# Optimization experiments

Measured on AMD Instinct MI355X. Metric: run time of the kernel, lower is better.

## Reference

```python
import jax, jax.numpy as jnp
import numpy as np

PAD_IDX = 0  # tgt_dict.stoi[PAD_WORD]
TLEN, BATCH, SLEN, CVOCAB = 64, 32, 128, 64
D, VOCAB = 1024, 50257


def setup_inputs() -> dict:
    key = jax.random.key(0)
    ks = jax.random.split(key, 7)
    hidden = jax.random.normal(ks[0], (TLEN * BATCH, D), dtype=jnp.float32)
    # attention distribution over source positions (rows sum to 1)
    attn = jax.nn.softmax(jax.random.normal(ks[1], (TLEN * BATCH, SLEN), dtype=jnp.float32), axis=-1)
    # sparse one-hot indicator: each source position maps to one extended-vocab slot
    src_idx = jax.random.randint(ks[2], (SLEN, BATCH), 0, CVOCAB)
    src_map = jax.nn.one_hot(src_idx, CVOCAB, dtype=jnp.float32)  # [slen, batch, cvocab]
    W_gen = jax.random.normal(ks[3], (VOCAB, D), dtype=jnp.float32) * 0.02
    b_gen = jnp.zeros((VOCAB,), dtype=jnp.float32)
    W_copy = jax.random.normal(ks[4], (1, D), dtype=jnp.float32) * 0.02
    b_copy = jnp.zeros((1,), dtype=jnp.float32)
    return {"hidden": hidden, "attn": attn, "src_map": src_map,
            "W_gen": W_gen, "b_gen": b_gen, "W_copy": W_copy, "b_copy": b_copy}


def reference(hidden, attn, src_map, W_gen, b_gen, W_copy, b_copy):
    slen, batch, cvocab = src_map.shape
    # p_softmax over tgt dict, with PAD masked to -inf before softmax
    logits = hidden @ W_gen.T + b_gen                      # [N, vocab]
    logits = logits.at[:, PAD_IDX].set(-jnp.inf)
    prob = jax.nn.softmax(logits, axis=-1)                 # [N, vocab]
    # copy gate p(z)
    p_copy = jax.nn.sigmoid(hidden @ W_copy.T + b_copy)    # [N, 1]
    out_prob = prob * (1.0 - p_copy)                       # [N, vocab]
    mul_attn = attn * p_copy                               # [N, slen]
    # torch flattening is tlen-major: view(-1, batch, slen) -> [tlen, batch, slen]
    mul_attn = mul_attn.reshape(-1, batch, slen)
    # bmm against sparse one-hot indicator: [tlen,batch,slen] x [slen,batch,cvocab]
    copy_prob = jnp.einsum('tbs,sbc->tbc', mul_attn, src_map)
    copy_prob = copy_prob.reshape(-1, cvocab)              # [N, cvocab]
    return jnp.concatenate([out_prob, copy_prob], axis=1)  # [N, vocab+cvocab]
```

## Files before the change

### kernel.cpp

```cpp
#include <hip/hip_runtime.h>
#include <hip/hip_bf16.h>

#define VOCAB 50257
#define CVOCAB 64
#define OUTW (VOCAB + CVOCAB)
#define DDIM 1024
#define NROWS 2048
#define SLEN 128
#define NVT 393
#define NVT2 197
#define VOCABP2 (NVT2 * 256)
#define RSTRIDE 72

typedef __attribute__((ext_vector_type(8))) short bf16x8;
typedef __attribute__((ext_vector_type(4))) float f32x4;
typedef __attribute__((ext_vector_type(2))) unsigned long long u64x2;
typedef __attribute__((ext_vector_type(8))) int i32x8;

#if __has_builtin(__builtin_amdgcn_mfma_scale_f32_16x16x128_f8f6f4)
#define MXOK 1
#else
#define MXOK 0
#endif

__device__ __forceinline__ unsigned short f2bf(float f) {
  union { float f; unsigned u; } x; x.f = f;
  unsigned r = x.u + 0x7FFFu + ((x.u >> 16) & 1u);
  return (unsigned short)(r >> 16);
}

__device__ __forceinline__ unsigned char f2e4m3(float f) {
  unsigned u = __float_as_uint(f);
  unsigned s = (u >> 24) & 0x80u;
  float a = __uint_as_float(u & 0x7FFFFFFFu);
  if (!(a < 448.f)) a = 448.f;
  if (a < 0.015625f) {
    int q = (int)rintf(a * 512.f);
    return (unsigned char)(s | (unsigned)q);
  }
  unsigned b = __float_as_uint(a);
  unsigned lsb = (b >> 20) & 1u;
  b += 0x0007FFFFu + lsb;
  int e = (int)((b >> 23) & 0xFF) - 127;
  unsigned m = (b >> 20) & 7u;
  return (unsigned char)(s | ((unsigned)(e + 7) << 3) | m);
}

__device__ __forceinline__ unsigned pack_e4m3x4(float a, float b, float c, float d) {
#if __has_builtin(__builtin_amdgcn_cvt_pk_fp8_f32)
  int r = __builtin_amdgcn_cvt_pk_fp8_f32(a, b, 0, false);
  r = __builtin_amdgcn_cvt_pk_fp8_f32(c, d, r, true);
  return (unsigned)r;
#else
  return (unsigned)f2e4m3(a) | ((unsigned)f2e4m3(b) << 8) |
         ((unsigned)f2e4m3(c) << 16) | ((unsigned)f2e4m3(d) << 24);
#endif
}

__device__ __forceinline__ i32x8 mk8(unsigned long long x0, unsigned long long x1,
                                     unsigned long long x2, unsigned long long x3) {
  i32x8 r;
  r[0] = (int)x0; r[1] = (int)(x0 >> 32);
  r[2] = (int)x1; r[3] = (int)(x1 >> 32);
  r[4] = (int)x2; r[5] = (int)(x2 >> 32);
  r[6] = (int)x3; r[7] = (int)(x3 >> 32);
  return r;
}

__global__ __launch_bounds__(256) void k_pcopy(const float* __restrict__ hidden,
                                               const float* __restrict__ Wc,
                                               const float* __restrict__ bc,
                                               float* __restrict__ pc) {
  int n = blockIdx.x * 4 + (threadIdx.x >> 6);
  int lane = threadIdx.x & 63;
  const float4* h = (const float4*)(hidden + (size_t)n * DDIM);
  const float4* w = (const float4*)Wc;
  float s = 0.0f;
  for (int i = lane; i < DDIM / 4; i += 64) {
    float4 a = h[i], b = w[i];
    s += a.x * b.x + a.y * b.y + a.z * b.z + a.w * b.w;
  }
  #pragma unroll
  for (int m = 1; m < 64; m <<= 1) s += __shfl_xor(s, m);
  if (lane == 0) pc[n] = 1.0f / (1.0f + __expf(-(s + bc[0])));
}

__global__ __launch_bounds__(256) void k_cvtA8(const float* __restrict__ src,
                                               unsigned char* __restrict__ dst) {
  int i = blockIdx.x * 256 + threadIdx.x;
  float4 v = *(const float4*)(src + (size_t)i * 4);
  *(unsigned*)(dst + (size_t)i * 4) = pack_e4m3x4(v.x, v.y, v.z, v.w);
}

__global__ __launch_bounds__(256) void k_cvtW8(const float* __restrict__ Wg,
                                               unsigned char* __restrict__ Wf8) {
  int row = blockIdx.x;
  int t = threadIdx.x;
  unsigned r = 0;
  if (row < VOCAB) {
    float4 v = *(const float4*)(Wg + (size_t)row * DDIM + t * 4);
    r = pack_e4m3x4(v.x * 64.f, v.y * 64.f, v.z * 64.f, v.w * 64.f);
  }
  *(unsigned*)(Wf8 + (size_t)row * DDIM + t * 4) = r;
}

template<int OM>
__global__ __launch_bounds__(512, 2) void k_gemm8(const unsigned char* __restrict__ A,
                                                  const unsigned char* __restrict__ W,
                                                  const float* __restrict__ bg,
                                                  float* __restrict__ out,
                                                  unsigned short* __restrict__ ebuf,
                                                  float* __restrict__ partial) {
  __shared__ __align__(16) unsigned char sA[2][256 * RSTRIDE];
  __shared__ __align__(16) unsigned char sB[2][256 * RSTRIDE];
  __shared__ float psum[1024];

  const int tid = threadIdx.x;
  const int lane = tid & 63;
  const int w = tid >> 6;
  const int wr = w >> 2, wn = w & 3;
  const int lrow = lane & 15, kgrp = lane >> 4;

  int swz = (blockIdx.x & 7) * 197 + (blockIdx.x >> 3);
  const int mt = swz & 7, vt = swz >> 3;
  const int m0 = mt * 256;
  const int v0 = vt * 256;

  const int srow = tid >> 2, scol = (tid & 3) * 16;
  const size_t gA0 = (size_t)(m0 + srow) * DDIM + scol;
  const size_t gA1 = gA0 + (size_t)128 * DDIM;
  const size_t gW0 = (size_t)(v0 + srow) * DDIM + scol;
  const size_t gW1 = gW0 + (size_t)128 * DDIM;
  const int l0 = srow * RSTRIDE + scol;
  const int l1 = l0 + 128 * RSTRIDE;

  int aoff[8], boff[4];
  #pragma unroll
  for (int rf = 0; rf < 8; rf++)
    aoff[rf] = (wr * 128 + rf * 16 + lrow) * RSTRIDE + kgrp * 8;
  #pragma unroll
  for (int cf = 0; cf < 4; cf++)
    boff[cf] = (wn * 64 + cf * 16 + lrow) * RSTRIDE + kgrp * 8;

  f32x4 acc[8][4] = {};

  u64x2 ra0, ra1, rb0, rb1;
  unsigned long long ae0[8], ae1[8], be0[4], be1[4];

  #define LOADT(t) { \
    ra0 = *(const u64x2*)(A + gA0 + (t) * 64); \
    ra1 = *(const u64x2*)(A + gA1 + (t) * 64); \
    rb0 = *(const u64x2*)(W + gW0 + (t) * 64); \
    rb1 = *(const u64x2*)(W + gW1 + (t) * 64); \
  }
  #define WRITET(buf) { \
    unsigned char* da = &sA[buf][0]; \
    unsigned char* db = &sB[buf][0]; \
    *(unsigned long long*)(da + l0)     = ra0[0]; \
    *(unsigned long long*)(da + l0 + 8) = ra0[1]; \
    *(unsigned long long*)(da + l1)     = ra1[0]; \
    *(unsigned long long*)(da + l1 + 8) = ra1[1]; \
    *(unsigned long long*)(db + l0)     = rb0[0]; \
    *(unsigned long long*)(db + l0 + 8) = rb0[1]; \
    *(unsigned long long*)(db + l1)     = rb1[0]; \
    *(unsigned long long*)(db + l1 + 8) = rb1[1]; \
  }

  LOADT(0);
  WRITET(0);
  asm volatile("s_waitcnt lgkmcnt(0)" ::: "memory");
  __builtin_amdgcn_s_barrier();

  for (int tp = 0; tp < 8; tp++) {
    const int t = tp * 2;
    {
      LOADT(t + 1);
      const unsigned char* pa = &sA[0][0];
      const unsigned char* pb = &sB[0][0];
      #pragma unroll
      for (int rf = 0; rf < 8; rf++) {
        ae0[rf] = *(const unsigned long long*)(pa + aoff[rf]);
        ae1[rf] = *(const unsigned long long*)(pa + aoff[rf] + 32);
      }
      #pragma unroll
      for (int cf = 0; cf < 4; cf++) {
        be0[cf] = *(const unsigned long long*)(pb + boff[cf]);
        be1[cf] = *(const unsigned long long*)(pb + boff[cf] + 32);
      }
      WRITET(1);
      asm volatile("s_waitcnt lgkmcnt(0)" ::: "memory");
      __builtin_amdgcn_s_barrier();
    }
    {
      const bool pf = (tp < 7);
      if (pf) LOADT(t + 2);
      const unsigned char* pa = &sA[1][0];
      const unsigned char* pb = &sB[1][0];
      unsigned long long ao0[8], ao1[8], bo0[4], bo1[4];
      #pragma unroll
      for (int rf = 0; rf < 8; rf++) {
        ao0[rf] = *(const unsigned long long*)(pa + aoff[rf]);
        ao1[rf] = *(const unsigned long long*)(pa + aoff[rf] + 32);
      }
      #pragma unroll
      for (int cf = 0; cf < 4; cf++) {
        bo0[cf] = *(const unsigned long long*)(pb + boff[cf]);
        bo1[cf] = *(const unsigned long long*)(pb + boff[cf] + 32);
      }
      __builtin_amdgcn_s_setprio(1);
#if MXOK
      i32x8 bfr[4];
      #pragma unroll
      for (int cf = 0; cf < 4; cf++)
        bfr[cf] = mk8(be0[cf], be1[cf], bo0[cf], bo1[cf]);
      #pragma unroll
      for (int rf = 0; rf < 8; rf++) {
        i32x8 afr = mk8(ae0[rf], ae1[rf], ao0[rf], ao1[rf]);
        #pragma unroll
        for (int cf = 0; cf < 4; cf++)
          acc[rf][cf] = __builtin_amdgcn_mfma_scale_f32_16x16x128_f8f6f4(
              afr, bfr[cf], acc[rf][cf], 0, 0,
              0, 0x7F7F7F7F, 0, 0x7F7F7F7F);
      }
#else
      #pragma unroll
      for (int rf = 0; rf < 8; rf++)
        #pragma unroll
        for (int cf = 0; cf < 4; cf++) {
          acc[rf][cf] = __builtin_amdgcn_mfma_f32_16x16x32_fp8_fp8(
              (long)ae0[rf], (long)be0[cf], acc[rf][cf], 0, 0, 0);
          acc[rf][cf] = __builtin_amdgcn_mfma_f32_16x16x32_fp8_fp8(
              (long)ae1[rf], (long)be1[cf], acc[rf][cf], 0, 0, 0);
          acc[rf][cf] = __builtin_amdgcn_mfma_f32_16x16x32_fp8_fp8(
              (long)ao0[rf], (long)bo0[cf], acc[rf][cf], 0, 0, 0);
          acc[rf][cf] = __builtin_amdgcn_mfma_f32_16x16x32_fp8_fp8(
              (long)ao1[rf], (long)bo1[cf], acc[rf][cf], 0, 0, 0);
        }
#endif
      __builtin_amdgcn_s_setprio(0);
      if (pf) {
        WRITET(0);
        asm volatile("s_waitcnt lgkmcnt(0)" ::: "memory");
        __builtin_amdgcn_s_barrier();
      }
    }
  }
  #undef LOADT
  #undef WRITET

  const float INV = 0.015625f;
  float bgv[4];
  int vcol[4];
  #pragma unroll
  for (int cf = 0; cf < 4; cf++) {
    vcol[cf] = v0 + wn * 64 + cf * 16 + lrow;
    bgv[cf] = (vcol[cf] < VOCAB) ? bg[vcol[cf]] : 0.0f;
  }
  #pragma unroll
  for (int a = 0; a < 8; a++) {
    #pragma unroll
    for (int r = 0; r < 4; r++) {
      int lr = wr * 128 + a * 16 + kgrp * 4 + r;
      int row = m0 + lr;
      float s = 0.0f;
      #pragma unroll
      for (int cf = 0; cf < 4; cf++) {
        int v = vcol[cf];
        float e = 0.0f;
        if (v < VOCAB && v != 0) e = __expf(acc[a][cf][r] * INV + bgv[cf]);
        if (OM == 0) {
          if (v < VOCAB) out[(size_t)row * OUTW + v] = e;
        } else {
          if (v < VOCAB) ebuf[(size_t)row * VOCABP2 + v + (row & 3)] = f2bf(e);
        }
        s += e;
      }
      s += __shfl_xor(s, 1); s += __shfl_xor(s, 2);
      s += __shfl_xor(s, 4); s += __shfl_xor(s, 8);
      if (lrow == 0) psum[wn * 256 + lr] = s;
    }
  }
  __syncthreads();
  if (tid < 256)
    partial[(size_t)vt * NROWS + m0 + tid] =
        psum[tid] + psum[256 + tid] + psum[512 + tid] + psum[768 + tid];
}

__global__ __launch_bounds__(256) void k_gemm(const float* __restrict__ hidden,
                                              const float* __restrict__ Wg,
                                              const float* __restrict__ bg,
                                              float* __restrict__ out,
                                              float* __restrict__ partial) {
  __shared__ __align__(16) unsigned char smemA[128 * 64 * 2];
  __shared__ __align__(16) unsigned char smemB[128 * 64 * 2];
  __shared__ float psum[2][128];

  const int tid = threadIdx.x;
  const int lane = tid & 63;
  const int wid = tid >> 6;
  const int wr = wid >> 1, wc = wid & 1;
  const int lrow = lane & 15, kgrp = lane >> 4;
  const int m0 = blockIdx.x * 128;
  const int vt = blockIdx.y;
  const int v0 = vt * 128;

  f32x4 acc[4][4] = {};

  for (int kt = 0; kt < 16; kt++) {
    const int k0 = kt * 64;
    #pragma unroll
    for (int i = 0; i < 8; i++) {
      int f = i * 256 + tid;
      int row = f >> 4;
      int kq = (f & 15) << 2;
      float4 v = *(const float4*)(hidden + (size_t)(m0 + row) * DDIM + k0 + kq);
      ushort4 h;
      h.x = f2bf(v.x); h.y = f2bf(v.y); h.z = f2bf(v.z); h.w = f2bf(v.w);
      *(ushort4*)(smemA + row * 128 + ((kq << 1) ^ ((row & 7) << 4))) = h;
    }
    #pragma unroll
    for (int i = 0; i < 8; i++) {
      int f = i * 256 + tid;
      int row = f >> 4;
      int kq = (f & 15) << 2;
      float4 v = make_float4(0.f, 0.f, 0.f, 0.f);
      if (v0 + row < VOCAB)
        v = *(const float4*)(Wg + (size_t)(v0 + row) * DDIM + k0 + kq);
      ushort4 h;
      h.x = f2bf(v.x); h.y = f2bf(v.y); h.z = f2bf(v.z); h.w = f2bf(v.w);
      *(ushort4*)(smemB + row * 128 + ((kq << 1) ^ ((row & 7) << 4))) = h;
    }
    __syncthreads();
    #pragma unroll
    for (int ks = 0; ks < 2; ks++) {
      const int kb = (ks * 32 + kgrp * 8) * 2;
      bf16x8 af[4], bfr[4];
      #pragma unroll
      for (int i = 0; i < 4; i++) {
        int ar = wr * 64 + i * 16 + lrow;
        af[i] = *(const bf16x8*)(smemA + ar * 128 + (kb ^ ((ar & 7) << 4)));
        int br = wc * 64 + i * 16 + lrow;
        bfr[i] = *(const bf16x8*)(smemB + br * 128 + (kb ^ ((br & 7) << 4)));
      }
      #pragma unroll
      for (int i = 0; i < 4; i++)
        #pragma unroll
        for (int j = 0; j < 4; j++)
          acc[i][j] = __builtin_amdgcn_mfma_f32_16x16x32_bf16(af[i], bfr[j], acc[i][j], 0, 0, 0);
    }
    __syncthreads();
  }

  float bgv[4];
  int vcol[4];
  #pragma unroll
  for (int j = 0; j < 4; j++) {
    vcol[j] = v0 + wc * 64 + j * 16 + lrow;
    bgv[j] = (vcol[j] < VOCAB) ? bg[vcol[j]] : 0.0f;
  }
  #pragma unroll
  for (int i = 0; i < 4; i++) {
    #pragma unroll
    for (int r = 0; r < 4; r++) {
      int row = m0 + wr * 64 + i * 16 + kgrp * 4 + r;
      float s = 0.0f;
      #pragma unroll
      for (int j = 0; j < 4; j++) {
        int v = vcol[j];
        float e = 0.0f;
        if (v < VOCAB && v != 0) e = __expf(acc[i][j][r] + bgv[j]);
        if (v < VOCAB) out[(size_t)row * OUTW + v] = e;
        s += e;
      }
      s += __shfl_xor(s, 1); s += __shfl_xor(s, 2);
      s += __shfl_xor(s, 4); s += __shfl_xor(s, 8);
      if ((lane & 15) == 0) psum[wc][wr * 64 + i * 16 + kgrp * 4 + r] = s;
    }
  }
  __syncthreads();
  if (tid < 128)
    partial[(size_t)vt * NROWS + m0 + tid] = psum[0][tid] + psum[1][tid];
}

__global__ __launch_bounds__(256) void k_reduce(const float* __restrict__ partial,
                                                const float* __restrict__ pc,
                                                float* __restrict__ scale, int nvt) {
  int row = blockIdx.x * 8 + (threadIdx.x >> 5);
  int sl = threadIdx.x & 31;
  float s = 0.0f;
  for (int t = sl; t < nvt; t += 32) s += partial[(size_t)t * NROWS + row];
  s += __shfl_xor(s, 1); s += __shfl_xor(s, 2); s += __shfl_xor(s, 4);
  s += __shfl_xor(s, 8); s += __shfl_xor(s, 16);
  if (sl == 0) scale[row] = (1.0f - pc[row]) / s;
}

__global__ __launch_bounds__(256) void k_scale(float* __restrict__ out,
                                               const float* __restrict__ scale) {
  int n = blockIdx.x;
  float sc = scale[n];
  size_t base = (size_t)n * OUTW;
  int off = (int)((4 - (base & 3)) & 3);
  for (int c = threadIdx.x; c < off; c += 256) out[base + c] *= sc;
  int nv = (VOCAB - off) >> 2;
  f32x4* p = (f32x4*)(out + base + off);
  for (int i = threadIdx.x; i < nv; i += 256) {
    f32x4 v = p[i];
    v *= sc;
    __builtin_nontemporal_store(v, &p[i]);
  }
  for (int c = off + (nv << 2) + threadIdx.x; c < VOCAB; c += 256) out[base + c] *= sc;
}

__global__ __launch_bounds__(256) void k_scale2(const unsigned short* __restrict__ ebuf,
                                                const float* __restrict__ scale,
                                                float* __restrict__ out) {
  int n = blockIdx.x;
  float sc = scale[n];
  const int shift = n & 3;
  const int off = (4 - shift) & 3;
  const unsigned short* er = ebuf + (size_t)n * VOCABP2 + shift;
  float* orow = out + (size_t)n * OUTW;
  for (int c = threadIdx.x; c < off; c += 256)
    orow[c] = __uint_as_float((unsigned)er[c] << 16) * sc;
  int nv = (VOCAB - off) >> 2;
  for (int i = threadIdx.x; i < nv; i += 256) {
    int c = off + i * 4;
    ushort4 v = *(const ushort4*)(er + c);
    f32x4 f;
    f.x = __uint_as_float((unsigned)v.x << 16) * sc;
    f.y = __uint_as_float((unsigned)v.y << 16) * sc;
    f.z = __uint_as_float((unsigned)v.z << 16) * sc;
    f.w = __uint_as_float((unsigned)v.w << 16) * sc;
    __builtin_nontemporal_store(f, (f32x4*)(orow + c));
  }
  for (int c = off + (nv << 2) + threadIdx.x; c < VOCAB; c += 256)
    orow[c] = __uint_as_float((unsigned)er[c] << 16) * sc;
}

__global__ __launch_bounds__(64) void k_copy(const float* __restrict__ attn,
                                             const float* __restrict__ src_map,
                                             const float* __restrict__ pc,
                                             float* __restrict__ out) {
  int n = blockIdx.x;
  int c = threadIdx.x;
  int b = n & 31;
  __shared__ float arow[SLEN];
  arow[c] = attn[(size_t)n * SLEN + c];
  arow[c + 64] = attn[(size_t)n * SLEN + 64 + c];
  __syncthreads();
  float s = 0.0f;
  for (int sp = 0; sp < SLEN; sp++)
    s += arow[sp] * src_map[((size_t)sp * 32 + b) * CVOCAB + c];
  out[(size_t)n * OUTW + VOCAB + c] = s * pc[n];
}

extern "C" void kernel_launch(void* const* d_in, const int* in_sizes, int n_in,
                              void* d_out, int out_size, void* d_ws, size_t ws_size,
                              hipStream_t stream) {
  const float* hidden = (const float*)d_in[0];
  const float* attn   = (const float*)d_in[1];
  const float* srcmap = (const float*)d_in[2];
  const float* Wg     = (const float*)d_in[3];
  const float* bg     = (const float*)d_in[4];
  const float* Wc     = (const float*)d_in[5];
  const float* bc     = (const float*)d_in[6];
  float* out = (float*)d_out;

  char* ws = (char*)d_ws;
  float* pc      = (float*)ws;
  float* scale   = (float*)(ws + 8192);
  float* partial = (float*)(ws + 16384);
  size_t partEnd = 16384 + (size_t)NVT * NROWS * 4;
  unsigned char* A8 = (unsigned char*)(ws + partEnd);
  size_t aEnd = partEnd + (size_t)NROWS * DDIM;
  unsigned char* W8 = (unsigned char*)(ws + aEnd);
  size_t wEnd = aEnd + (size_t)VOCABP2 * DDIM;
  unsigned short* ebuf = (unsigned short*)(ws + wEnd);
  size_t need1 = wEnd;
  size_t need2 = wEnd + (size_t)NROWS * VOCABP2 * 2;

  k_pcopy<<<NROWS / 4, 256, 0, stream>>>(hidden, Wc, bc, pc);
  if (ws_size >= need1) {
    k_cvtA8<<<(NROWS * DDIM / 4) / 256, 256, 0, stream>>>(hidden, A8);
    k_cvtW8<<<VOCABP2, 256, 0, stream>>>(Wg, W8);
    if (ws_size >= need2) {
      k_gemm8<1><<<8 * NVT2, 512, 0, stream>>>(A8, W8, bg, out, ebuf, partial);
      k_reduce<<<NROWS / 8, 256, 0, stream>>>(partial, pc, scale, NVT2);
      k_scale2<<<NROWS, 256, 0, stream>>>(ebuf, scale, out);
    } else {
      k_gemm8<0><<<8 * NVT2, 512, 0, stream>>>(A8, W8, bg, out, ebuf, partial);
      k_reduce<<<NROWS / 8, 256, 0, stream>>>(partial, pc, scale, NVT2);
      k_scale<<<NROWS, 256, 0, stream>>>(out, scale);
    }
  } else {
    k_gemm<<<dim3(NROWS / 128, NVT), 256, 0, stream>>>(hidden, Wg, bg, out, partial);
    k_reduce<<<NROWS / 8, 256, 0, stream>>>(partial, pc, scale, NVT);
    k_scale<<<NROWS, 256, 0, stream>>>(out, scale);
  }
  k_copy<<<NROWS, 64, 0, stream>>>(attn, srcmap, pc, out);
}
```

Measured before the change: 409.4 us.

## Load GEMM tiles directly into LDS with XOR-swizzled layout

Replaces the register-staged global load and LDS write path in the fp8 GEMM with direct global-to-LDS loads (global_load_lds, 16 bytes). Because those loads write LDS contiguously per thread, the padded row stride is dropped in favour of an XOR swizzle applied to the global source column and to the fragment read offsets, to avoid bank conflicts. This removes the VGPR staging and ds_write instructions and may free registers. In exchange it waits on vmcnt before each barrier, which can expose global latency, and it relies on the swizzle mapping being correct.

```diff
diff --git a/kernel.cpp b/kernel.cpp
--- a/kernel.cpp
+++ b/kernel.cpp
@@ -10,11 +10,9 @@
 #define NVT 393
 #define NVT2 197
 #define VOCABP2 (NVT2 * 256)
-#define RSTRIDE 72
 
 typedef __attribute__((ext_vector_type(8))) short bf16x8;
 typedef __attribute__((ext_vector_type(4))) float f32x4;
-typedef __attribute__((ext_vector_type(2))) unsigned long long u64x2;
 typedef __attribute__((ext_vector_type(8))) int i32x8;
 
 #if __has_builtin(__builtin_amdgcn_mfma_scale_f32_16x16x128_f8f6f4)
@@ -65,6 +63,11 @@
   r[4] = (int)x2; r[5] = (int)(x2 >> 32);
   r[6] = (int)x3; r[7] = (int)(x3 >> 32);
   return r;
+}
+
+__device__ __forceinline__ void gload_lds16(const void* g, void* l) {
+  __builtin_amdgcn_global_load_lds((const __attribute__((address_space(1))) void*)g,
+                                   (__attribute__((address_space(3))) void*)l, 16, 0, 0);
 }
 
 __global__ __launch_bounds__(256) void k_pcopy(const float* __restrict__ hidden,
@@ -111,8 +114,8 @@
                                                   float* __restrict__ out,
                                                   unsigned short* __restrict__ ebuf,
                                                   float* __restrict__ partial) {
-  __shared__ __align__(16) unsigned char sA[2][256 * RSTRIDE];
-  __shared__ __align__(16) unsigned char sB[2][256 * RSTRIDE];
+  __shared__ __align__(16) unsigned char sA[2][16384];
+  __shared__ __align__(16) unsigned char sB[2][16384];
   __shared__ float psum[1024];
 
   const int tid = threadIdx.x;
@@ -126,86 +129,74 @@
   const int m0 = mt * 256;
   const int v0 = vt * 256;
 
-  const int srow = tid >> 2, scol = (tid & 3) * 16;
-  const size_t gA0 = (size_t)(m0 + srow) * DDIM + scol;
+  const int srow = tid >> 2;
+  const int c_sw = (tid & 3) ^ ((srow >> 1) & 3);
+  const size_t gA0 = (size_t)(m0 + srow) * DDIM + c_sw * 16;
   const size_t gA1 = gA0 + (size_t)128 * DDIM;
-  const size_t gW0 = (size_t)(v0 + srow) * DDIM + scol;
+  const size_t gW0 = (size_t)(v0 + srow) * DDIM + c_sw * 16;
   const size_t gW1 = gW0 + (size_t)128 * DDIM;
-  const int l0 = srow * RSTRIDE + scol;
-  const int l1 = l0 + 128 * RSTRIDE;
 
   int aoff[8], boff[4];
   #pragma unroll
-  for (int rf = 0; rf < 8; rf++)
-    aoff[rf] = (wr * 128 + rf * 16 + lrow) * RSTRIDE + kgrp * 8;
-  #pragma unroll
-  for (int cf = 0; cf < 4; cf++)
-    boff[cf] = (wn * 64 + cf * 16 + lrow) * RSTRIDE + kgrp * 8;
+  for (int rf = 0; rf < 8; rf++) {
+    int row = wr * 128 + rf * 16 + lrow;
+    aoff[rf] = row * 64 + (((kgrp >> 1) ^ ((row >> 1) & 3)) << 4) + ((kgrp & 1) << 3);
+  }
+  #pragma unroll
+  for (int cf = 0; cf < 4; cf++) {
+    int row = wn * 64 + cf * 16 + lrow;
+    boff[cf] = row * 64 + (((kgrp >> 1) ^ ((row >> 1) & 3)) << 4) + ((kgrp & 1) << 3);
+  }
 
   f32x4 acc[8][4] = {};
-
-  u64x2 ra0, ra1, rb0, rb1;
   unsigned long long ae0[8], ae1[8], be0[4], be1[4];
 
-  #define LOADT(t) { \
-    ra0 = *(const u64x2*)(A + gA0 + (t) * 64); \
-    ra1 = *(const u64x2*)(A + gA1 + (t) * 64); \
-    rb0 = *(const u64x2*)(W + gW0 + (t) * 64); \
-    rb1 = *(const u64x2*)(W + gW1 + (t) * 64); \
-  }
-  #define WRITET(buf) { \
-    unsigned char* da = &sA[buf][0]; \
-    unsigned char* db = &sB[buf][0]; \
-    *(unsigned long long*)(da + l0)     = ra0[0]; \
-    *(unsigned long long*)(da + l0 + 8) = ra0[1]; \
-    *(unsigned long long*)(da + l1)     = ra1[0]; \
-    *(unsigned long long*)(da + l1 + 8) = ra1[1]; \
-    *(unsigned long long*)(db + l0)     = rb0[0]; \
-    *(unsigned long long*)(db + l0 + 8) = rb0[1]; \
-    *(unsigned long long*)(db + l1)     = rb1[0]; \
-    *(unsigned long long*)(db + l1 + 8) = rb1[1]; \
-  }
-
-  LOADT(0);
-  WRITET(0);
-  asm volatile("s_waitcnt lgkmcnt(0)" ::: "memory");
+  #define GLOAD(t) { \
+    int _b = (t) & 1; \
+    gload_lds16(A + gA0 + (t) * 64, &sA[_b][(size_t)tid * 16]); \
+    gload_lds16(A + gA1 + (t) * 64, &sA[_b][(size_t)(512 + tid) * 16]); \
+    gload_lds16(W + gW0 + (t) * 64, &sB[_b][(size_t)tid * 16]); \
+    gload_lds16(W + gW1 + (t) * 64, &sB[_b][(size_t)(512 + tid) * 16]); \
+  }
+
+  GLOAD(0);
+  asm volatile("s_waitcnt vmcnt(0)" ::: "memory");
   __builtin_amdgcn_s_barrier();
 
   for (int tp = 0; tp < 8; tp++) {
     const int t = tp * 2;
     {
-      LOADT(t + 1);
+      GLOAD(t + 1);
       const unsigned char* pa = &sA[0][0];
       const unsigned char* pb = &sB[0][0];
       #pragma unroll
       for (int rf = 0; rf < 8; rf++) {
         ae0[rf] = *(const unsigned long long*)(pa + aoff[rf]);
-        ae1[rf] = *(const unsigned long long*)(pa + aoff[rf] + 32);
+        ae1[rf] = *(const unsigned long long*)(pa + (aoff[rf] ^ 32));
       }
       #pragma unroll
       for (int cf = 0; cf < 4; cf++) {
         be0[cf] = *(const unsigned long long*)(pb + boff[cf]);
-        be1[cf] = *(const unsigned long long*)(pb + boff[cf] + 32);
-      }
-      WRITET(1);
-      asm volatile("s_waitcnt lgkmcnt(0)" ::: "memory");
+        be1[cf] = *(const unsigned long long*)(pb + (boff[cf] ^ 32));
+      }
+      asm volatile("s_waitcnt vmcnt(0)" ::: "memory");
       __builtin_amdgcn_s_barrier();
     }
     {
       const bool pf = (tp < 7);
-      if (pf) LOADT(t + 2);
+      if (pf) GLOAD(t + 2);
       const unsigned char* pa = &sA[1][0];
       const unsigned char* pb = &sB[1][0];
       unsigned long long ao0[8], ao1[8], bo0[4], bo1[4];
       #pragma unroll
       for (int rf = 0; rf < 8; rf++) {
         ao0[rf] = *(const unsigned long long*)(pa + aoff[rf]);
-        ao1[rf] = *(const unsigned long long*)(pa + aoff[rf] + 32);
+        ao1[rf] = *(const unsigned long long*)(pa + (aoff[rf] ^ 32));
       }
       #pragma unroll
       for (int cf = 0; cf < 4; cf++) {
         bo0[cf] = *(const unsigned long long*)(pb + boff[cf]);
-        bo1[cf] = *(const unsigned long long*)(pb + boff[cf] + 32);
+        bo1[cf] = *(const unsigned long long*)(pb + (boff[cf] ^ 32));
       }
       __builtin_amdgcn_s_setprio(1);
 #if MXOK
@@ -239,14 +230,12 @@
 #endif
       __builtin_amdgcn_s_setprio(0);
       if (pf) {
-        WRITET(0);
-        asm volatile("s_waitcnt lgkmcnt(0)" ::: "memory");
+        asm volatile("s_waitcnt vmcnt(0)" ::: "memory");
         __builtin_amdgcn_s_barrier();
       }
     }
   }
-  #undef LOADT
-  #undef WRITET
+  #undef GLOAD
 
   const float INV = 0.015625f;
   float bgv[4];
```

Measured after the change: 425.5 us. 1.04x slower.
